# Performance work log

Measured on AMD Instinct MI355X. Metric: run time of the kernel, lower is better.

The kernel has to match this reference:

```python
import jax, jax.numpy as jnp
import numpy as np


def setup_inputs() -> dict:
    key = jax.random.key(0)
    k1, k2, k3, k4, k5 = jax.random.split(key, 5)
    B, L, D = 8, 4096, 64
    return {
        "Q": jax.random.normal(k1, (B, L, D), dtype=jnp.float32),
        "K": jax.random.normal(k2, (B, L, D), dtype=jnp.float32),
        "V": jax.random.normal(k3, (B, L, D), dtype=jnp.float32),
        "sent_embed_slice": jax.random.normal(k4, (B, D), dtype=jnp.float32),
        "proj": jax.random.normal(k5, (D, D), dtype=jnp.float32),  # fixed phi projection (M, d)
        "qkv_size": 64,
        "masked": 1,
    }


def _phi(X, proj, M):
    # X: (B, L, d). Original applies phi per timestep slice x = X[:, t, :] of shape (B, d)
    # phi(x) = (1/sqrt(M)) * exp(-0.5 * ||x||_F) * exp(proj @ x), Frobenius norm over the (B, d) slice.
    logits = jnp.einsum("bld,md->blm", X, proj)            # (B, L, M)
    scale = jnp.exp(-0.5 * jnp.sqrt(jnp.sum(X * X, axis=(0, 2))))  # per-timestep scalar, (L,)
    return jnp.exp(logits) * scale[None, :, None] / jnp.sqrt(jnp.asarray(M, jnp.float32))


def reference(Q, K, V, sent_embed_slice, proj, qkv_size, masked):
    M = qkv_size
    phi_q = _phi(Q, proj, M)  # (B, L, M)
    phi_k = _phi(K, proj, M)  # (B, L, M)
    if masked:
        # causal running sums: KV_t = sum_{j<=t} phi_k_j outer V_j ; N_t = sum_{j<=t} phi_k_j
        KV = jnp.cumsum(phi_k[:, :, :, None] * V[:, :, None, :], axis=1)  # (B, L, M, D)
        Nc = jnp.cumsum(phi_k, axis=1)                                    # (B, L, M)
        num = jnp.einsum("blm,blmd->bld", phi_q, KV)
        r = jnp.einsum("blm,blm->bl", phi_q, Nc)
        return num / (r + jnp.sign(r) * 1e-6)[:, :, None]
    else:
        KV = jnp.einsum("blm,bld->bmd", phi_k, V)     # (B, M, D)
        Ns = jnp.sum(phi_k, axis=1)                    # (B, M); broadcast over D like torch norm_sum
        num = jnp.einsum("blm,bmd->bld", phi_q, KV)
        r = jnp.einsum("blm,bm->bl", phi_q, Ns)
        return num / r[:, :, None]
```

## Files before the change

### kernel.cpp

```cpp
#include <hip/hip_runtime.h>
#include <math.h>

#define BB 8
#define LL 4096
#define DD 64
#define SS 64
#define NCHUNK 64
#define STATE 4160

typedef __attribute__((ext_vector_type(8))) short s16x8;
typedef __attribute__((ext_vector_type(8))) unsigned short u16x8;
typedef __attribute__((ext_vector_type(4))) float f32x4;

#define MFMA(a, b, c) __builtin_amdgcn_mfma_f32_16x16x32_bf16((a), (b), (c), 0, 0, 0)

static __device__ __forceinline__ unsigned short f2bf(float x) {
  unsigned int u = __builtin_bit_cast(unsigned int, x);
  u += 0x7FFFu + ((u >> 16) & 1u);
  return (unsigned short)(u >> 16);
}
static __device__ __forceinline__ float bf2f(unsigned short h) {
  unsigned int u = ((unsigned int)h) << 16;
  return __builtin_bit_cast(float, u);
}


static __device__ __forceinline__ s16x8 ld_frag(const unsigned short* base, int row0, int ks) {
  const int lane = threadIdx.x & 63;
  const int r = row0 + (lane & 15);
  const int idx = r * 64 + ((ks * 32 + ((lane & 48) >> 1)) ^ ((r & 7) << 3));
  return *(const s16x8*)(base + idx);
}

static __device__ __forceinline__ void ldg_hl(const float* __restrict__ G, int row0, int ks,
                                              s16x8& h, s16x8& l) {
  const int lane = threadIdx.x & 63;
  const int r = row0 + (lane & 15);
  const int k0 = ks * 32 + ((lane & 48) >> 1);
  const float4 a = *(const float4*)(G + r * 64 + k0);
  const float4 b = *(const float4*)(G + r * 64 + k0 + 4);
  const float xs[8] = {a.x, a.y, a.z, a.w, b.x, b.y, b.z, b.w};
#pragma unroll
  for (int i = 0; i < 8; ++i) {
    const unsigned short hh = f2bf(xs[i]);
    h[i] = (short)hh;
    l[i] = (short)f2bf(xs[i] - bf2f(hh));
  }
}

static __device__ __forceinline__ s16x8 ldg_bf(const unsigned short* __restrict__ G, int row0, int ks) {
  const int lane = threadIdx.x & 63;
  const int r = row0 + (lane & 15);
  const int k0 = ks * 32 + ((lane & 48) >> 1);
  return *(const s16x8*)(G + r * 64 + k0);
}

static __device__ __forceinline__ void ldg_vt_hl(const float* __restrict__ V, int row0, int ks,
                                                 s16x8& h, s16x8& l) {
  const int lane = threadIdx.x & 63;
  const int d = row0 + (lane & 15);
  const int t0 = ks * 32 + ((lane & 48) >> 1);
#pragma unroll
  for (int i = 0; i < 8; ++i) {
    const float v = V[(t0 + i) * 64 + d];
    const unsigned short hh = f2bf(v);
    h[i] = (short)hh;
    l[i] = (short)f2bf(v - bf2f(hh));
  }
}

static __device__ __forceinline__ void phi_store_row(unsigned short* dst, const f32x4* acc,
                                                     const float* sc, int w) {
  const int lane = threadIdx.x & 63;
#pragma unroll
  for (int ri = 0; ri < 4; ++ri) {
    const int t = w * 16 + ((lane & 48) >> 2) + ri;
#pragma unroll
    for (int ct = 0; ct < 4; ++ct) {
      const int m = ct * 16 + (lane & 15);
      dst[t * 64 + (m ^ ((t & 7) << 3))] = f2bf(__expf(acc[ct][ri]) * sc[ri]);
    }
  }
}

static __device__ __forceinline__ void phi_store_col(unsigned short* dst, const f32x4* acc,
                                                     const float* sc, int w) {
  const int lane = threadIdx.x & 63;
#pragma unroll
  for (int ri = 0; ri < 4; ++ri) {
    const int t = w * 16 + ((lane & 48) >> 2) + ri;
#pragma unroll
    for (int ct = 0; ct < 4; ++ct) {
      const int m = ct * 16 + (lane & 15);
      dst[m * 64 + (t ^ ((m & 7) << 3))] = f2bf(__expf(acc[ct][ri]) * sc[ri]);
    }
  }
}

__global__ __launch_bounds__(256) void k_scales(const float* __restrict__ Q,
                                                const float* __restrict__ K,
                                                float* __restrict__ ws) {
  const int t = blockIdx.x * 4 + (threadIdx.x >> 6);
  const int lane = threadIdx.x & 63;
  const int b = lane >> 3;
  const int d0 = (lane & 7) * 8;
  const size_t base = (size_t)b * (LL * DD) + (size_t)t * DD + d0;
  float sq = 0.f, sk = 0.f;
#pragma unroll
  for (int k = 0; k < 8; ++k) {
    const float q = Q[base + k]; sq += q * q;
    const float kk = K[base + k]; sk += kk * kk;
  }
#pragma unroll
  for (int off = 32; off; off >>= 1) {
    sq += __shfl_xor(sq, off);
    sk += __shfl_xor(sk, off);
  }
  if (lane == 0) {
    ws[t]      = expf(-0.5f * sqrtf(sq));
    ws[LL + t] = expf(-0.5f * sqrtf(sk));
  }
}

__global__ __launch_bounds__(256) void k_phi_sums(const float* __restrict__ Qg,
                                                  const float* __restrict__ Kg,
                                                  const float* __restrict__ Vg,
                                                  const float* __restrict__ proj,
                                                  const float* __restrict__ ws,
                                                  float* __restrict__ states,
                                                  unsigned short* __restrict__ phiQg,
                                                  unsigned short* __restrict__ phiKg) {
  __shared__ unsigned short PQ[4096];
  __shared__ unsigned short PKr[4096];
  __shared__ unsigned short PKc[4096];
  const int tid = threadIdx.x;
  const int lane = tid & 63;
  const int w = tid >> 6;
  const int bc = blockIdx.x;
  const int b = bc >> 6;
  const int c = bc & (NCHUNK - 1);
  const int t0 = c * SS;
  const size_t tileBase = ((size_t)b * LL + t0) * DD;
  float* stc = states + ((size_t)b * NCHUNK + c) * (size_t)STATE;
  unsigned short* pqT = phiQg + (size_t)bc * 4096;
  unsigned short* pkT = phiKg + (size_t)bc * 4096;

  s16x8 vh[2], vl[2];
#pragma unroll
  for (int ks = 0; ks < 2; ++ks) ldg_vt_hl(Vg + tileBase, w * 16, ks, vh[ks], vl[ks]);

  s16x8 ph[4][2], pl[4][2];
#pragma unroll
  for (int ct = 0; ct < 4; ++ct)
#pragma unroll
    for (int ks = 0; ks < 2; ++ks) ldg_hl(proj, ct * 16, ks, ph[ct][ks], pl[ct][ks]);

  float scq[4], sck[4];
#pragma unroll
  for (int ri = 0; ri < 4; ++ri) {
    const int trow = w * 16 + ((lane & 48) >> 2) + ri;
    scq[ri] = ws[t0 + trow] * 0.125f;
    sck[ri] = ws[LL + t0 + trow] * 0.125f;
  }

  {
    s16x8 qh[2], ql[2];
#pragma unroll
    for (int ks = 0; ks < 2; ++ks) ldg_hl(Qg + tileBase, w * 16, ks, qh[ks], ql[ks]);
    f32x4 acc[4] = {};
#pragma unroll
    for (int ct = 0; ct < 4; ++ct)
#pragma unroll
      for (int ks = 0; ks < 2; ++ks) {
        acc[ct] = MFMA(qh[ks], ph[ct][ks], acc[ct]);
        acc[ct] = MFMA(qh[ks], pl[ct][ks], acc[ct]);
        acc[ct] = MFMA(ql[ks], ph[ct][ks], acc[ct]);
      }
    phi_store_row(PQ, acc, scq, w);
  }
  {
    s16x8 kh[2], kl[2];
#pragma unroll
    for (int ks = 0; ks < 2; ++ks) ldg_hl(Kg + tileBase, w * 16, ks, kh[ks], kl[ks]);
    f32x4 acc[4] = {};
#pragma unroll
    for (int ct = 0; ct < 4; ++ct)
#pragma unroll
      for (int ks = 0; ks < 2; ++ks) {
        acc[ct] = MFMA(kh[ks], ph[ct][ks], acc[ct]);
        acc[ct] = MFMA(kh[ks], pl[ct][ks], acc[ct]);
        acc[ct] = MFMA(kl[ks], ph[ct][ks], acc[ct]);
      }
    phi_store_row(PKr, acc, sck, w);
    phi_store_col(PKc, acc, sck, w);
  }
  __syncthreads();

  {
    const int r0 = tid >> 3;
    const int c0 = (tid & 7) * 8;
#pragma unroll
    for (int it = 0; it < 2; ++it) {
      const int r = r0 + it * 32;
      const int sidx = r * 64 + (c0 ^ ((r & 7) << 3));
      *(u16x8*)(pqT + r * 64 + c0) = *(const u16x8*)(PQ + sidx);
      *(u16x8*)(pkT + r * 64 + c0) = *(const u16x8*)(PKr + sidx);
    }
  }
  {
    const int m = tid >> 2, q = tid & 3;
    float s = 0.f;
#pragma unroll
    for (int p = 0; p < 2; ++p) {
      const int tt = q * 16 + p * 8;
      const u16x8 vv = *(const u16x8*)(PKc + m * 64 + (tt ^ ((m & 7) << 3)));
#pragma unroll
      for (int i = 0; i < 8; ++i) s += bf2f(vv[i]);
    }
    s += __shfl_xor(s, 1);
    s += __shfl_xor(s, 2);
    if (q == 0) stc[4096 + m] = s;
  }
  {
    f32x4 acc[4] = {};
#pragma unroll
    for (int ct = 0; ct < 4; ++ct)
#pragma unroll
      for (int ks = 0; ks < 2; ++ks) {
        const s16x8 bp = ld_frag(PKc, ct * 16, ks);
        acc[ct] = MFMA(vh[ks], bp, acc[ct]);
        acc[ct] = MFMA(vl[ks], bp, acc[ct]);
      }
#pragma unroll
    for (int ri = 0; ri < 4; ++ri) {
      const int d = w * 16 + ((lane & 48) >> 2) + ri;
#pragma unroll
      for (int ct = 0; ct < 4; ++ct) {
        stc[d * 64 + ct * 16 + (lane & 15)] = acc[ct][ri];
      }
    }
  }
}

__global__ __launch_bounds__(256) void k_prefix1(const float* __restrict__ states,
                                                 float* __restrict__ tmp) {
  const int e = blockIdx.x * 256 + threadIdx.x;
  if (e >= BB * 8 * STATE) return;
  const int b = e / (8 * STATE);
  const int r = e % (8 * STATE);
  const int g = r / STATE;
  const int el = r % STATE;
  const float* p = states + ((size_t)b * NCHUNK + g * 8) * STATE + el;
  float s = 0.f;
#pragma unroll
  for (int i = 0; i < 8; ++i) s += p[(size_t)i * STATE];
  tmp[((size_t)b * 8 + g) * STATE + el] = s;
}

__global__ __launch_bounds__(256) void k_prefix2(float* __restrict__ states,
                                                 const float* __restrict__ tmp) {
  const int e = blockIdx.x * 256 + threadIdx.x;
  if (e >= BB * 8 * STATE) return;
  const int b = e / (8 * STATE);
  const int r = e % (8 * STATE);
  const int g = r / STATE;
  const int el = r % STATE;
  float run = 0.f;
  for (int g2 = 0; g2 < g; ++g2) run += tmp[((size_t)b * 8 + g2) * STATE + el];
  float* p = states + ((size_t)b * NCHUNK + g * 8) * STATE + el;
#pragma unroll
  for (int i = 0; i < 8; ++i) {
    const float v = p[(size_t)i * STATE];
    p[(size_t)i * STATE] = run;
    run += v;
  }
}

__global__ __launch_bounds__(256) void k_out(const float* __restrict__ Vg,
                                             const unsigned short* __restrict__ phiQg,
                                             const unsigned short* __restrict__ phiKg,
                                             const float* __restrict__ states,
                                             float* __restrict__ out) {
  __shared__ unsigned short E[4096];
  const int tid = threadIdx.x;
  const int lane = tid & 63;
  const int w = tid >> 6;
  const int bc = blockIdx.x;
  const int b = bc >> 6;
  const int c = bc & (NCHUNK - 1);
  const int t0 = c * SS;
  const size_t tileBase = ((size_t)b * LL + t0) * DD;
  const float* st = states + ((size_t)b * NCHUNK + c) * (size_t)STATE;
  const unsigned short* pqT = phiQg + (size_t)bc * 4096;
  const unsigned short* pkT = phiKg + (size_t)bc * 4096;

  s16x8 aq[2];
#pragma unroll
  for (int ks = 0; ks < 2; ++ks) aq[ks] = ldg_bf(pqT, w * 16, ks);

  float rsI[4];
  {
    f32x4 accA[4] = {};
#pragma unroll
    for (int ct = 0; ct < 4; ++ct)
#pragma unroll
      for (int ks = 0; ks < 2; ++ks)
        accA[ct] = MFMA(aq[ks], ldg_bf(pkT, ct * 16, ks), accA[ct]);
#pragma unroll
    for (int ri = 0; ri < 4; ++ri) {
      const int t = w * 16 + ((lane & 48) >> 2) + ri;
      float part = 0.f;
#pragma unroll
      for (int ct = 0; ct < 4; ++ct) {
        const int j = ct * 16 + (lane & 15);
        const float a = (j <= t) ? accA[ct][ri] : 0.f;
        const unsigned short ah = f2bf(a);
        part += bf2f(ah);
        E[t * 64 + (j ^ ((t & 7) << 3))] = ah;
      }
#pragma unroll
      for (int off = 1; off < 16; off <<= 1) part += __shfl_xor(part, off);
      rsI[ri] = part;
    }
  }
  __syncthreads();

  {
    s16x8 aA[2];
#pragma unroll
    for (int ks = 0; ks < 2; ++ks) aA[ks] = ld_frag(E, w * 16, ks);
    f32x4 acc[4] = {};
#pragma unroll
    for (int ct = 0; ct < 4; ++ct) {
      s16x8 vth[2], vtl[2], kvh[2], kvl[2];
#pragma unroll
      for (int ks = 0; ks < 2; ++ks) {
        ldg_vt_hl(Vg + tileBase, ct * 16, ks, vth[ks], vtl[ks]);
        ldg_hl(st, ct * 16, ks, kvh[ks], kvl[ks]);
      }
#pragma unroll
      for (int ks = 0; ks < 2; ++ks) {
        acc[ct] = MFMA(aA[ks], vth[ks], acc[ct]);
        acc[ct] = MFMA(aA[ks], vtl[ks], acc[ct]);
        acc[ct] = MFMA(aq[ks], kvh[ks], acc[ct]);
        acc[ct] = MFMA(aq[ks], kvl[ks], acc[ct]);
      }
    }
    float rsp = 0.f;
    const float* Np = st + 4096;
#pragma unroll
    for (int ks = 0; ks < 2; ++ks) {
      const int m0 = ks * 32 + ((lane & 48) >> 1);
      const float4 n0 = *(const float4*)(Np + m0);
      const float4 n1 = *(const float4*)(Np + m0 + 4);
      const float nn[8] = {n0.x, n0.y, n0.z, n0.w, n1.x, n1.y, n1.z, n1.w};
#pragma unroll
      for (int i = 0; i < 8; ++i) rsp += bf2f((unsigned short)aq[ks][i]) * nn[i];
    }
    rsp += __shfl_xor(rsp, 16);
    rsp += __shfl_xor(rsp, 32);
#pragma unroll
    for (int ri = 0; ri < 4; ++ri) {
      const float r = rsI[ri] + __shfl(rsp, ((lane & 48) >> 2) + ri);
      const float inv = 1.f / (r + copysignf(1e-6f, r));
      const int t = w * 16 + ((lane & 48) >> 2) + ri;
#pragma unroll
      for (int ct = 0; ct < 4; ++ct) {
        out[tileBase + t * 64 + ct * 16 + (lane & 15)] = acc[ct][ri] * inv;
      }
    }
  }
}

extern "C" void kernel_launch(void* const* d_in, const int* in_sizes, int n_in,
                              void* d_out, int out_size, void* d_ws, size_t ws_size,
                              hipStream_t stream) {
  (void)in_sizes; (void)n_in; (void)out_size; (void)ws_size;
  const float* Q    = (const float*)d_in[0];
  const float* K    = (const float*)d_in[1];
  const float* V    = (const float*)d_in[2];
  const float* proj = (const float*)d_in[4];
  float* out = (float*)d_out;
  float* ws  = (float*)d_ws;
  float* states = ws + 2 * LL;
  const size_t statesFloats = (size_t)BB * NCHUNK * STATE;
  float* tmp = states + statesFloats;
  const size_t tmpFloats = (size_t)BB * 8 * STATE;
  unsigned short* phiQg = (unsigned short*)(tmp + tmpFloats);
  unsigned short* phiKg = phiQg + (size_t)BB * NCHUNK * 4096;

  hipLaunchKernelGGL(k_scales, dim3(LL / 4), dim3(256), 0, stream, Q, K, ws);
  hipLaunchKernelGGL(k_phi_sums, dim3(BB * NCHUNK), dim3(256), 0, stream,
                     Q, K, V, proj, ws, states, phiQg, phiKg);
  hipLaunchKernelGGL(k_prefix1, dim3((BB * 8 * STATE + 255) / 256), dim3(256), 0, stream, states, tmp);
  hipLaunchKernelGGL(k_prefix2, dim3((BB * 8 * STATE + 255) / 256), dim3(256), 0, stream, states, tmp);
  hipLaunchKernelGGL(k_out, dim3(BB * NCHUNK), dim3(256), 0, stream,
                     V, phiQg, phiKg, states, out);
}
```

Baseline: 41.14 us.

## Recompute phi(Q),phi(K) in output kernel and stage V/state tiles through LDS

Stops writing bf16 phi(Q) and phi(K) tiles to global memory in the chunk-sum kernel and instead recomputes them with MFMA inside the output kernel. It also stages the V tile (transposed, split into hi/lo bf16) and the chunk state into LDS instead of doing strided global gathers per fragment. This removes a global round trip and the uncoalesced V-transpose loads. In exchange it adds MFMA work and much more shared memory per block (about 64KB), which can lower occupancy.

```diff
diff --git a/kernel.cpp b/kernel.cpp
--- a/kernel.cpp
+++ b/kernel.cpp
@@ -48,13 +48,6 @@
   }
 }
 
-static __device__ __forceinline__ s16x8 ldg_bf(const unsigned short* __restrict__ G, int row0, int ks) {
-  const int lane = threadIdx.x & 63;
-  const int r = row0 + (lane & 15);
-  const int k0 = ks * 32 + ((lane & 48) >> 1);
-  return *(const s16x8*)(G + r * 64 + k0);
-}
-
 static __device__ __forceinline__ void ldg_vt_hl(const float* __restrict__ V, int row0, int ks,
                                                  s16x8& h, s16x8& l) {
   const int lane = threadIdx.x & 63;
@@ -97,6 +90,61 @@
   }
 }
 
+static __device__ __forceinline__ void stage_hl(unsigned short* __restrict__ Sh,
+                                                unsigned short* __restrict__ Sl,
+                                                const float* __restrict__ src, int tid) {
+#pragma unroll
+  for (int it = 0; it < 2; ++it) {
+    const int g = tid + it * 256;
+    const int row = g >> 3;
+    const int c0 = (g & 7) * 8;
+    const float4 x0 = *(const float4*)(src + row * 64 + c0);
+    const float4 x1 = *(const float4*)(src + row * 64 + c0 + 4);
+    const float xs[8] = {x0.x, x0.y, x0.z, x0.w, x1.x, x1.y, x1.z, x1.w};
+    u16x8 h, l;
+#pragma unroll
+    for (int k = 0; k < 8; ++k) {
+      const unsigned short hh = f2bf(xs[k]);
+      h[k] = hh;
+      l[k] = f2bf(xs[k] - bf2f(hh));
+    }
+    const int idx = row * 64 + (c0 ^ ((row & 7) << 3));
+    *(u16x8*)(Sh + idx) = h;
+    *(u16x8*)(Sl + idx) = l;
+  }
+}
+
+static __device__ __forceinline__ void stage_vfull(float* __restrict__ F, const float* __restrict__ src,
+                                                   int tid) {
+#pragma unroll
+  for (int it = 0; it < 4; ++it) {
+    const int g = tid + it * 256;
+    const int row = g >> 4;
+    const int col = (g & 15) * 4;
+    *(float4*)(F + row * 64 + col) = *(const float4*)(src + row * 64 + col);
+  }
+}
+
+static __device__ __forceinline__ void vtrans_half(unsigned short* __restrict__ Gh,
+                                                   unsigned short* __restrict__ Hl,
+                                                   const float* __restrict__ F, int tid, int half) {
+  const int d = tid & 63;
+  const int tb = (tid >> 6) * 8;
+  float v[8];
+#pragma unroll
+  for (int k = 0; k < 8; ++k) v[k] = F[(tb + k) * 64 + d];
+  u16x8 hh, ll;
+#pragma unroll
+  for (int k = 0; k < 8; ++k) {
+    const unsigned short h = f2bf(v[k]);
+    hh[k] = h;
+    ll[k] = f2bf(v[k] - bf2f(h));
+  }
+  const int idx = d * 64 + ((half * 32 + tb) ^ ((d & 7) << 3));
+  *(u16x8*)(Gh + idx) = hh;
+  *(u16x8*)(Hl + idx) = ll;
+}
+
 __global__ __launch_bounds__(256) void k_scales(const float* __restrict__ Q,
                                                 const float* __restrict__ K,
                                                 float* __restrict__ ws) {
@@ -122,16 +170,11 @@
   }
 }
 
-__global__ __launch_bounds__(256) void k_phi_sums(const float* __restrict__ Qg,
-                                                  const float* __restrict__ Kg,
-                                                  const float* __restrict__ Vg,
-                                                  const float* __restrict__ proj,
-                                                  const float* __restrict__ ws,
-                                                  float* __restrict__ states,
-                                                  unsigned short* __restrict__ phiQg,
-                                                  unsigned short* __restrict__ phiKg) {
-  __shared__ unsigned short PQ[4096];
-  __shared__ unsigned short PKr[4096];
+__global__ __launch_bounds__(256) void k_chunk_sums(const float* __restrict__ Kg,
+                                                    const float* __restrict__ Vg,
+                                                    const float* __restrict__ proj,
+                                                    const float* __restrict__ ws,
+                                                    float* __restrict__ states) {
   __shared__ unsigned short PKc[4096];
   const int tid = threadIdx.x;
   const int lane = tid & 63;
@@ -142,8 +185,6 @@
   const int t0 = c * SS;
   const size_t tileBase = ((size_t)b * LL + t0) * DD;
   float* stc = states + ((size_t)b * NCHUNK + c) * (size_t)STATE;
-  unsigned short* pqT = phiQg + (size_t)bc * 4096;
-  unsigned short* pkT = phiKg + (size_t)bc * 4096;
 
   s16x8 vh[2], vl[2];
 #pragma unroll
@@ -155,29 +196,13 @@
 #pragma unroll
     for (int ks = 0; ks < 2; ++ks) ldg_hl(proj, ct * 16, ks, ph[ct][ks], pl[ct][ks]);
 
-  float scq[4], sck[4];
+  float sck[4];
 #pragma unroll
   for (int ri = 0; ri < 4; ++ri) {
     const int trow = w * 16 + ((lane & 48) >> 2) + ri;
-    scq[ri] = ws[t0 + trow] * 0.125f;
     sck[ri] = ws[LL + t0 + trow] * 0.125f;
   }
 
-  {
-    s16x8 qh[2], ql[2];
-#pragma unroll
-    for (int ks = 0; ks < 2; ++ks) ldg_hl(Qg + tileBase, w * 16, ks, qh[ks], ql[ks]);
-    f32x4 acc[4] = {};
-#pragma unroll
-    for (int ct = 0; ct < 4; ++ct)
-#pragma unroll
-      for (int ks = 0; ks < 2; ++ks) {
-        acc[ct] = MFMA(qh[ks], ph[ct][ks], acc[ct]);
-        acc[ct] = MFMA(qh[ks], pl[ct][ks], acc[ct]);
-        acc[ct] = MFMA(ql[ks], ph[ct][ks], acc[ct]);
-      }
-    phi_store_row(PQ, acc, scq, w);
-  }
   {
     s16x8 kh[2], kl[2];
 #pragma unroll
@@ -191,22 +216,10 @@
         acc[ct] = MFMA(kh[ks], pl[ct][ks], acc[ct]);
         acc[ct] = MFMA(kl[ks], ph[ct][ks], acc[ct]);
       }
-    phi_store_row(PKr, acc, sck, w);
     phi_store_col(PKc, acc, sck, w);
   }
   __syncthreads();
 
-  {
-    const int r0 = tid >> 3;
-    const int c0 = (tid & 7) * 8;
-#pragma unroll
-    for (int it = 0; it < 2; ++it) {
-      const int r = r0 + it * 32;
-      const int sidx = r * 64 + (c0 ^ ((r & 7) << 3));
-      *(u16x8*)(pqT + r * 64 + c0) = *(const u16x8*)(PQ + sidx);
-      *(u16x8*)(pkT + r * 64 + c0) = *(const u16x8*)(PKr + sidx);
-    }
-  }
   {
     const int m = tid >> 2, q = tid & 3;
     float s = 0.f;
@@ -276,12 +289,18 @@
   }
 }
 
-__global__ __launch_bounds__(256) void k_out(const float* __restrict__ Vg,
-                                             const unsigned short* __restrict__ phiQg,
-                                             const unsigned short* __restrict__ phiKg,
+__global__ __launch_bounds__(256) void k_out(const float* __restrict__ Qg,
+                                             const float* __restrict__ Kg,
+                                             const float* __restrict__ Vg,
+                                             const float* __restrict__ proj,
+                                             const float* __restrict__ ws,
                                              const float* __restrict__ states,
                                              float* __restrict__ out) {
-  __shared__ unsigned short E[4096];
+  __shared__ unsigned short PB[4096];
+  __shared__ unsigned short PK[4096];
+  __shared__ unsigned short VT0[4096], VT1[4096];
+  __shared__ unsigned short KV0[4096], KV1[4096];
+  __shared__ float F[4096];
   const int tid = threadIdx.x;
   const int lane = tid & 63;
   const int w = tid >> 6;
@@ -291,12 +310,61 @@
   const int t0 = c * SS;
   const size_t tileBase = ((size_t)b * LL + t0) * DD;
   const float* st = states + ((size_t)b * NCHUNK + c) * (size_t)STATE;
-  const unsigned short* pqT = phiQg + (size_t)bc * 4096;
-  const unsigned short* pkT = phiKg + (size_t)bc * 4096;
-
+
+  stage_vfull(F, Vg + tileBase, tid);
+  stage_hl(KV0, KV1, st, tid);
+
+  s16x8 ph[4][2], pl[4][2];
+#pragma unroll
+  for (int ct = 0; ct < 4; ++ct)
+#pragma unroll
+    for (int ks = 0; ks < 2; ++ks) ldg_hl(proj, ct * 16, ks, ph[ct][ks], pl[ct][ks]);
+
+  float scq[4], sck[4];
+#pragma unroll
+  for (int ri = 0; ri < 4; ++ri) {
+    const int trow = w * 16 + ((lane & 48) >> 2) + ri;
+    scq[ri] = ws[t0 + trow] * 0.125f;
+    sck[ri] = ws[LL + t0 + trow] * 0.125f;
+  }
+
+  {
+    s16x8 kh[2], kl[2];
+#pragma unroll
+    for (int ks = 0; ks < 2; ++ks) ldg_hl(Kg + tileBase, w * 16, ks, kh[ks], kl[ks]);
+    f32x4 acc[4] = {};
+#pragma unroll
+    for (int ct = 0; ct < 4; ++ct)
+#pragma unroll
+      for (int ks = 0; ks < 2; ++ks) {
+        acc[ct] = MFMA(kh[ks], ph[ct][ks], acc[ct]);
+        acc[ct] = MFMA(kh[ks], pl[ct][ks], acc[ct]);
+        acc[ct] = MFMA(kl[ks], ph[ct][ks], acc[ct]);
+      }
+    phi_store_row(PK, acc, sck, w);
+  }
   s16x8 aq[2];
-#pragma unroll
-  for (int ks = 0; ks < 2; ++ks) aq[ks] = ldg_bf(pqT, w * 16, ks);
+  {
+    s16x8 qh[2], ql[2];
+#pragma unroll
+    for (int ks = 0; ks < 2; ++ks) ldg_hl(Qg + tileBase, w * 16, ks, qh[ks], ql[ks]);
+    f32x4 acc[4] = {};
+#pragma unroll
+    for (int ct = 0; ct < 4; ++ct)
+#pragma unroll
+      for (int ks = 0; ks < 2; ++ks) {
+        acc[ct] = MFMA(qh[ks], ph[ct][ks], acc[ct]);
+        acc[ct] = MFMA(qh[ks], pl[ct][ks], acc[ct]);
+        acc[ct] = MFMA(ql[ks], ph[ct][ks], acc[ct]);
+      }
+    phi_store_row(PB, acc, scq, w);
+#pragma unroll
+    for (int ks = 0; ks < 2; ++ks) aq[ks] = ld_frag(PB, w * 16, ks);
+  }
+  __syncthreads();
+
+  vtrans_half(VT0, VT1, F, tid, 0);
+  vtrans_half(VT0, VT1, F + 32 * 64, tid, 1);
 
   float rsI[4];
   {
@@ -305,7 +373,7 @@
     for (int ct = 0; ct < 4; ++ct)
 #pragma unroll
       for (int ks = 0; ks < 2; ++ks)
-        accA[ct] = MFMA(aq[ks], ldg_bf(pkT, ct * 16, ks), accA[ct]);
+        accA[ct] = MFMA(aq[ks], ld_frag(PK, ct * 16, ks), accA[ct]);
 #pragma unroll
     for (int ri = 0; ri < 4; ++ri) {
       const int t = w * 16 + ((lane & 48) >> 2) + ri;
@@ -316,7 +384,7 @@
         const float a = (j <= t) ? accA[ct][ri] : 0.f;
         const unsigned short ah = f2bf(a);
         part += bf2f(ah);
-        E[t * 64 + (j ^ ((t & 7) << 3))] = ah;
+        PB[t * 64 + (j ^ ((t & 7) << 3))] = ah;
       }
 #pragma unroll
       for (int off = 1; off < 16; off <<= 1) part += __shfl_xor(part, off);
@@ -328,22 +396,16 @@
   {
     s16x8 aA[2];
 #pragma unroll
-    for (int ks = 0; ks < 2; ++ks) aA[ks] = ld_frag(E, w * 16, ks);
+    for (int ks = 0; ks < 2; ++ks) aA[ks] = ld_frag(PB, w * 16, ks);
     f32x4 acc[4] = {};
 #pragma unroll
     for (int ct = 0; ct < 4; ++ct) {
-      s16x8 vth[2], vtl[2], kvh[2], kvl[2];
 #pragma unroll
       for (int ks = 0; ks < 2; ++ks) {
-        ldg_vt_hl(Vg + tileBase, ct * 16, ks, vth[ks], vtl[ks]);
-        ldg_hl(st, ct * 16, ks, kvh[ks], kvl[ks]);
-      }
-#pragma unroll
-      for (int ks = 0; ks < 2; ++ks) {
-        acc[ct] = MFMA(aA[ks], vth[ks], acc[ct]);
-        acc[ct] = MFMA(aA[ks], vtl[ks], acc[ct]);
-        acc[ct] = MFMA(aq[ks], kvh[ks], acc[ct]);
-        acc[ct] = MFMA(aq[ks], kvl[ks], acc[ct]);
+        acc[ct] = MFMA(aA[ks], ld_frag(VT0, ct * 16, ks), acc[ct]);
+        acc[ct] = MFMA(aA[ks], ld_frag(VT1, ct * 16, ks), acc[ct]);
+        acc[ct] = MFMA(aq[ks], ld_frag(KV0, ct * 16, ks), acc[ct]);
+        acc[ct] = MFMA(aq[ks], ld_frag(KV1, ct * 16, ks), acc[ct]);
       }
     }
     float rsp = 0.f;
@@ -385,15 +447,12 @@
   float* states = ws + 2 * LL;
   const size_t statesFloats = (size_t)BB * NCHUNK * STATE;
   float* tmp = states + statesFloats;
-  const size_t tmpFloats = (size_t)BB * 8 * STATE;
-  unsigned short* phiQg = (unsigned short*)(tmp + tmpFloats);
-  unsigned short* phiKg = phiQg + (size_t)BB * NCHUNK * 4096;
 
   hipLaunchKernelGGL(k_scales, dim3(LL / 4), dim3(256), 0, stream, Q, K, ws);
-  hipLaunchKernelGGL(k_phi_sums, dim3(BB * NCHUNK), dim3(256), 0, stream,
-                     Q, K, V, proj, ws, states, phiQg, phiKg);
+  hipLaunchKernelGGL(k_chunk_sums, dim3(BB * NCHUNK), dim3(256), 0, stream,
+                     K, V, proj, ws, states);
   hipLaunchKernelGGL(k_prefix1, dim3((BB * 8 * STATE + 255) / 256), dim3(256), 0, stream, states, tmp);
   hipLaunchKernelGGL(k_prefix2, dim3((BB * 8 * STATE + 255) / 256), dim3(256), 0, stream, states, tmp);
   hipLaunchKernelGGL(k_out, dim3(BB * NCHUNK), dim3(256), 0, stream,
-                     V, phiQg, phiKg, states, out);
-}
+                     Q, K, V, proj, ws, states, out);
+}
```

After: 40.21 us. 2.2% less time.
